# Kernel optimization log

Measured on AMD Instinct MI355X. Metric: run time of the kernel, lower is better.

The kernel has to match this reference:

```python
import jax, jax.numpy as jnp
import numpy as np

B, S, D = 24, 512, 512
H, HS, HSEL = 8, 1, 2
DK = D // H
DFF = 2048
NQ, NPID = 1000, 5000
NB = 2
NL = 3 * NB  # blocks_1 (NB) + blocks_2 (2*NB)
FC1, FC2 = 512, 256


def setup_inputs():
    key = jax.random.key(0)
    ks = jax.random.split(key, 32)
    def w(k, shape, scale=0.02):
        return jax.random.normal(k, shape, dtype=jnp.float32) * scale
    inp = {}
    inp['q_data'] = jax.random.randint(ks[0], (B, S), 0, NQ + 1)
    inp['target'] = jax.random.randint(ks[1], (B, S), 0, 2)
    inp['pid_data'] = jax.random.randint(ks[2], (B, S), 0, NPID + 1)
    # embedding tables (padding_idx=0 -> zero row)
    inp['q_embed_tab'] = w(ks[3], (NQ + 1, D)).at[0].set(0.0)
    inp['qa_embed_tab'] = w(ks[4], (3, D)).at[0].set(0.0)
    inp['q_diff_tab'] = w(ks[5], (NQ + 1, D)).at[0].set(0.0)
    inp['qa_diff_tab'] = w(ks[6], (2 * NQ + 1, D)).at[0].set(0.0)
    inp['pid_diff_tab'] = w(ks[7], (NPID + 1, 1)).at[0].set(0.0)
    # stacked per-layer transformer params, leading dim NL
    inp['Wq'] = w(ks[8], (NL, D, D)); inp['bq'] = jnp.zeros((NL, D), jnp.float32)
    inp['Wv'] = w(ks[9], (NL, D, D)); inp['bv'] = jnp.zeros((NL, D), jnp.float32)
    inp['Wg'] = w(ks[10], (NL, D, H - HS))  # router, no bias
    inp['Wo'] = w(ks[11], (NL, D, D)); inp['bo'] = jnp.zeros((NL, D), jnp.float32)
    inp['ln1_g'] = jnp.ones((NL, D), jnp.float32); inp['ln1_b'] = jnp.zeros((NL, D), jnp.float32)
    inp['W1'] = w(ks[12], (NL, D, DFF)); inp['b1'] = jnp.zeros((NL, DFF), jnp.float32)
    inp['W2'] = w(ks[13], (NL, DFF, D)); inp['b2'] = jnp.zeros((NL, D), jnp.float32)
    inp['ln2_g'] = jnp.ones((NL, D), jnp.float32); inp['ln2_b'] = jnp.zeros((NL, D), jnp.float32)
    # output MLP
    inp['ow1'] = w(ks[14], (2 * D, FC1)); inp['ob1'] = jnp.zeros((FC1,), jnp.float32)
    inp['ow2'] = w(ks[15], (FC1, FC2)); inp['ob2'] = jnp.zeros((FC2,), jnp.float32)
    inp['ow3'] = w(ks[16], (FC2, 1)); inp['ob3'] = jnp.zeros((1,), jnp.float32)
    return inp


def _ln(x, g, b, eps=1e-5):
    m = x.mean(-1, keepdims=True)
    v = ((x - m) ** 2).mean(-1, keepdims=True)
    return (x - m) * jax.lax.rsqrt(v + eps) * g + b


def _moh_attn(xq, xv, strict, Wq, bq, Wv, bv, Wg, Wo, bo):
    b, s, d = xq.shape
    ql = xq @ Wq + bq            # [b,s,D]; kq_same=True so k == q
    vl = xv @ Wv + bv
    q = ql.reshape(b, s, H, DK).transpose(0, 2, 1, 3)   # [b,H,s,dk]
    v = vl.reshape(b, s, H, DK).transpose(0, 2, 1, 3)
    scores = jnp.einsum('bhid,bhjd->bhij', q, q) / np.float32(np.sqrt(DK))
    i = jnp.arange(s)[:, None]
    j = jnp.arange(s)[None, :]
    allowed = (j < i) if strict else (j <= i)
    scores = jnp.where(allowed, scores, jnp.float32(-1e9))
    scores = scores.at[:, :, 0, :].set(0.0)  # pad_zero row -> uniform softmax
    # dynamic per-token head routing on the query projection
    gates = jax.nn.softmax(ql @ Wg, axis=-1)             # [b,s,H-HS]
    idx = jax.lax.top_k(gates, HSEL)[1]                  # [b,s,HSEL]
    dyn_mask = jax.nn.one_hot(idx, H - HS, dtype=gates.dtype).sum(-2)
    dyn_scores = gates * dyn_mask
    rmask = jnp.concatenate([jnp.ones((b, s, HS), gates.dtype), dyn_scores], -1).mean(1)  # [b,H]
    attn = jax.nn.softmax(scores, axis=-1)
    ctx = jnp.einsum('bhij,bhjd->bhid', attn, v) * rmask[:, :, None, None]
    ctx = ctx.transpose(0, 2, 1, 3).reshape(b, s, d)
    return ctx @ Wo + bo


def _block(xq, xv, strict, p):
    a = _moh_attn(xq, xv, strict, *p[:7])
    x = _ln(xq + a, p[7], p[8])
    f = jnp.maximum(x @ p[9] + p[10], 0.0) @ p[11] + p[12]
    return _ln(x + f, p[13], p[14])


def reference(q_data, target, pid_data, q_embed_tab, qa_embed_tab, q_diff_tab,
              qa_diff_tab, pid_diff_tab, Wq, bq, Wv, bv, Wg, Wo, bo,
              ln1_g, ln1_b, W1, b1, W2, b2, ln2_g, ln2_b,
              ow1, ob1, ow2, ob2, ow3, ob3):
    # Rasch-style embeddings (separate_qa=False, n_pid>0)
    q_emb = q_embed_tab[q_data]
    qa_emb = qa_embed_tab[target] + q_emb
    pid_emb = pid_diff_tab[pid_data]          # [B,S,1]
    qd = q_diff_tab[q_data]
    q_emb = q_emb + pid_emb * qd
    qa_emb = qa_emb + pid_emb * (qa_diff_tab[target] + qd)
    stacks = (Wq, bq, Wv, bv, Wg, Wo, bo, ln1_g, ln1_b, W1, b1, W2, b2, ln2_g, ln2_b)
    def P(i):
        return tuple(a[i] for a in stacks)
    y, x = qa_emb, q_emb
    for i in range(NB):                       # blocks_1: mask=1 (causal incl self)
        y = _block(y, y, False, P(i))
    flag = True
    for jj in range(2 * NB):                  # blocks_2: alternate self / cross-with-y
        i = NB + jj
        if flag:
            x = _block(x, x, False, P(i)); flag = False
        else:
            x = _block(x, y, True, P(i)); flag = True
    h = jnp.concatenate([x, q_emb], -1)       # [B,S,2D]
    h = jnp.maximum(h @ ow1 + ob1, 0.0)
    h = jnp.maximum(h @ ow2 + ob2, 0.0)
    return jax.nn.sigmoid((h @ ow3 + ob3)[..., 0])  # [B,S]
```

## Files before the change

### kernel.cpp

```cpp
#include <hip/hip_runtime.h>
#include <math.h>

typedef unsigned short u16;
typedef unsigned int   u32;
typedef __attribute__((ext_vector_type(8))) short short8;
typedef __attribute__((ext_vector_type(4))) float f32x4;
typedef __attribute__((ext_vector_type(16))) float f32x16;

#define Bb 24
#define Ss 512
#define Dd 512
#define DFFf 2048

__device__ __forceinline__ u16 f2b(float f) {
  u32 u = __float_as_uint(f);
  u32 r = (u + 0x7fffu + ((u >> 16) & 1u)) >> 16;
  return (u16)r;
}
__device__ __forceinline__ float b2f(u32 h) { return __uint_as_float(h << 16); }
__device__ __forceinline__ void cvt8(uint4 p, float* d) {
  d[0]=b2f(p.x&0xffffu); d[1]=b2f(p.x>>16);
  d[2]=b2f(p.y&0xffffu); d[3]=b2f(p.y>>16);
  d[4]=b2f(p.z&0xffffu); d[5]=b2f(p.z>>16);
  d[6]=b2f(p.w&0xffffu); d[7]=b2f(p.w>>16);
}

__global__ __launch_bounds__(256) void trans_kernel(
    const float* __restrict__ src, u16* __restrict__ dst, int K, int N,
    int dstLayer, int rowBase)
{
  __shared__ float t[32][33];
  int n0 = blockIdx.x*32, k0 = blockIdx.y*32;
  const float* s = src + (size_t)blockIdx.z*K*N;
  u16* d = dst + (size_t)blockIdx.z*dstLayer;
  int c = threadIdx.x & 31, r = threadIdx.x >> 5;
  #pragma unroll
  for (int rr=r; rr<32; rr+=8) t[rr][c] = s[(size_t)(k0+rr)*N + n0 + c];
  __syncthreads();
  #pragma unroll
  for (int rr=r; rr<32; rr+=8) d[(size_t)(rowBase + n0+rr)*K + k0 + c] = f2b(t[c][rr]);
}

__global__ __launch_bounds__(256) void embed_kernel(
    const int* __restrict__ q_data, const int* __restrict__ target, const int* __restrict__ pid_data,
    const float* __restrict__ q_tab, const float* __restrict__ qa_tab,
    const float* __restrict__ qd_tab, const float* __restrict__ qad_tab,
    const float* __restrict__ pid_tab,
    float* __restrict__ xb, float* __restrict__ yb,
    u16* __restrict__ qebf, u16* __restrict__ ybf)
{
  int t = blockIdx.x;
  int qi = q_data[t], tg = target[t], pi = pid_data[t];
  float pd = pid_tab[pi];
  const float* qe  = q_tab  + (size_t)qi*Dd;
  const float* qa  = qa_tab + (size_t)tg*Dd;
  const float* qd  = qd_tab + (size_t)qi*Dd;
  const float* qad = qad_tab+ (size_t)tg*Dd;
  size_t base = (size_t)t*Dd;
  for (int d = threadIdx.x; d < Dd; d += 256) {
    float e = qe[d], dv = qd[d];
    float qv  = e + pd*dv;
    float qav = qa[d] + e + pd*(qad[d] + dv);
    xb[base+d] = qv;  qebf[base+d] = f2b(qv);
    yb[base+d] = qav; ybf[base+d]  = f2b(qav);
  }
}

__global__ __launch_bounds__(256) void embed_x_kernel(
    const int* __restrict__ q_data, const int* __restrict__ pid_data,
    const float* __restrict__ q_tab, const float* __restrict__ qd_tab,
    const float* __restrict__ pid_tab, float* __restrict__ xb)
{
  int t = blockIdx.x;
  int qi = q_data[t], pi = pid_data[t];
  float pd = pid_tab[pi];
  const float* qe = q_tab + (size_t)qi*Dd;
  const float* qd = qd_tab + (size_t)qi*Dd;
  size_t base = (size_t)t*Dd;
  for (int d = threadIdx.x; d < Dd; d += 256)
    xb[base+d] = qe[d] + pd*qd[d];
}

__global__ __launch_bounds__(256) void gemm_bf16_kernel(
    const u16* __restrict__ A, const u16* __restrict__ A2,
    const u16* __restrict__ Wt,
    const float* __restrict__ bias, const float* __restrict__ bias2,
    float* __restrict__ Cf, u16* __restrict__ Cb, u16* __restrict__ Cb2,
    int M, int N, int K, int ldA, int ldw, int act, int nsplit, float* rinit)
{
  __shared__ u16 As[3][128*32];
  __shared__ u16 Bs[3][128*32];
  if (rinit && blockIdx.x==0 && blockIdx.y==0 && threadIdx.x < 192)
    rinit[threadIdx.x] = ((threadIdx.x & 7)==0) ? 1.f : 0.f;
  int bm = blockIdx.y*128, bn = blockIdx.x*128;
  int wv = threadIdx.x >> 6, lane = threadIdx.x & 63;
  int wm = (wv & 1)*64, wn = (wv >> 1)*64;

  const char* gAa[2]; const char* gAb[2]; const char* gB[2];
  u32 ldsOff[2];
  #pragma unroll
  for (int t=0; t<2; t++) {
    int flat = wv*128 + t*64 + lane;
    int row = flat >> 2, c = flat & 3;
    int sr = (row & 3) ^ ((row >> 2) & 3);
    int cb = ((c ^ sr) * 16);
    gAa[t] = (const char*)A + ((size_t)(bm+row)*ldA)*2 + cb;
    gAb[t] = A2 ? ((const char*)A2 + ((size_t)(bm+row)*ldA)*2 + cb) : gAa[t];
    gB[t]  = (const char*)Wt + ((size_t)(bn+row)*ldw)*2 + cb;
    ldsOff[t] = (u32)(wv*128 + t*64)*16;
  }
  int selLim = A2 ? 512 : 0x7fffffff;
  int kmask  = A2 ? 511 : 0x7fffffff;

  f32x16 acc[2][2];
  #pragma unroll
  for (int i=0;i<2;i++)
    #pragma unroll
    for (int j=0;j<2;j++)
      #pragma unroll
      for (int r=0;r<16;r++) acc[i][j][r] = 0.f;

  int m32 = lane & 31, hi = lane >> 5;
  int sL = (m32 & 3) ^ ((m32 >> 2) & 3);

  auto stage = [&](int kt, int buf) {
    int k0 = kt*32;
    size_t offA = (size_t)(k0 & kmask)*2;
    size_t offB = (size_t)k0*2;
    #pragma unroll
    for (int t=0; t<2; t++) {
      const char* sa = ((k0 < selLim) ? gAa[t] : gAb[t]) + offA;
      __builtin_amdgcn_global_load_lds(
          (const __attribute__((address_space(1))) void*)sa,
          (__attribute__((address_space(3))) void*)((char*)As[buf] + ldsOff[t]), 16, 0, 0);
      __builtin_amdgcn_global_load_lds(
          (const __attribute__((address_space(1))) void*)(gB[t] + offB),
          (__attribute__((address_space(3))) void*)((char*)Bs[buf] + ldsOff[t]), 16, 0, 0);
    }
  };

  int nk = K >> 5;
  stage(0, 0);
  stage(1, 1);
  for (int t=0; t<nk; t++) {
    if (t+1 < nk) {
      asm volatile("s_waitcnt vmcnt(4)\ns_barrier" ::: "memory");
    } else {
      asm volatile("s_waitcnt vmcnt(0)\ns_barrier" ::: "memory");
    }
    int buf = t % 3;
    const u16* Ab   = As[buf];
    const u16* Bbuf = Bs[buf];
    short8 af[2][2], bfr[2][2];
    #pragma unroll
    for (int i=0;i<2;i++)
      #pragma unroll
      for (int kk=0;kk<2;kk++) {
        af[i][kk]  = *(const short8*)(Ab   + (wm + i*32 + m32)*32 + (((kk*2+hi) ^ sL)*8));
        bfr[i][kk] = *(const short8*)(Bbuf + (wn + i*32 + m32)*32 + (((kk*2+hi) ^ sL)*8));
      }
    if (t+2 < nk) stage(t+2, (t+2) % 3);
    #pragma unroll
    for (int kk=0;kk<2;kk++)
      #pragma unroll
      for (int i=0;i<2;i++)
        #pragma unroll
        for (int j=0;j<2;j++)
          acc[i][j] = __builtin_amdgcn_mfma_f32_32x32x16_bf16(af[i][kk], bfr[j][kk], acc[i][j], 0, 0, 0);
  }

  int hisel = (bias2 != nullptr) && (bn >= nsplit);
  const float* bse = hisel ? bias2 : bias;
  u16* outb = hisel ? Cb2 : Cb;
  int cb0 = hisel ? nsplit : 0;
  int strideOut = bias2 ? nsplit : N;

  #pragma unroll
  for (int i=0;i<2;i++) {
    #pragma unroll
    for (int rg=0;rg<16;rg++) {
      int row = bm + wm + i*32 + (rg&3) + 8*(rg>>2) + 4*hi;
      #pragma unroll
      for (int j=0;j<2;j++) {
        int col = bn + wn + j*32 + m32;
        float v = acc[i][j][rg];
        if (bse) v += bse[col - cb0];
        if (act) v = fmaxf(v, 0.f);
        if (Cf)   Cf[(size_t)row*strideOut + col - cb0] = v;
        if (outb) outb[(size_t)row*strideOut + col - cb0] = f2b(v);
      }
    }
  }
}

__global__ __launch_bounds__(256) void add_ln_kernel(
    const float* __restrict__ xa, const u16* __restrict__ xbb,
    const float* __restrict__ g, const float* __restrict__ bta,
    float* __restrict__ outf, u16* __restrict__ outb)
{
  int row = blockIdx.x*4 + (threadIdx.x >> 6);
  int lane = threadIdx.x & 63;
  size_t base = (size_t)row*Dd + lane*8;
  float4 a0 = *(const float4*)(xa + base);
  float4 a1 = *(const float4*)(xa + base + 4);
  uint4  bb = *(const uint4*)(xbb + base);
  float v[8]; cvt8(bb, v);
  v[0]+=a0.x; v[1]+=a0.y; v[2]+=a0.z; v[3]+=a0.w;
  v[4]+=a1.x; v[5]+=a1.y; v[6]+=a1.z; v[7]+=a1.w;
  float s = ((v[0]+v[1])+(v[2]+v[3])) + ((v[4]+v[5])+(v[6]+v[7]));
  #pragma unroll
  for (int o=32;o;o>>=1) s += __shfl_xor(s, o);
  float mean = s * (1.f/512.f);
  float q = 0.f;
  #pragma unroll
  for (int k=0;k<8;k++) { float d = v[k]-mean; v[k]=d; q += d*d; }
  #pragma unroll
  for (int o=32;o;o>>=1) q += __shfl_xor(q, o);
  float inv = rsqrtf(q * (1.f/512.f) + 1e-5f);
  float4 g0 = *(const float4*)(g + lane*8);
  float4 g1 = *(const float4*)(g + lane*8 + 4);
  float4 b0 = *(const float4*)(bta + lane*8);
  float4 b1 = *(const float4*)(bta + lane*8 + 4);
  float r[8];
  r[0]=v[0]*inv*g0.x+b0.x; r[1]=v[1]*inv*g0.y+b0.y;
  r[2]=v[2]*inv*g0.z+b0.z; r[3]=v[3]*inv*g0.w+b0.w;
  r[4]=v[4]*inv*g1.x+b1.x; r[5]=v[5]*inv*g1.y+b1.y;
  r[6]=v[6]*inv*g1.z+b1.z; r[7]=v[7]*inv*g1.w+b1.w;
  float4 o0 = {r[0],r[1],r[2],r[3]};
  float4 o1 = {r[4],r[5],r[6],r[7]};
  *(float4*)(outf + base) = o0;
  *(float4*)(outf + base + 4) = o1;
  uint4 w;
  w.x = (u32)f2b(r[0]) | ((u32)f2b(r[1])<<16);
  w.y = (u32)f2b(r[2]) | ((u32)f2b(r[3])<<16);
  w.z = (u32)f2b(r[4]) | ((u32)f2b(r[5])<<16);
  w.w = (u32)f2b(r[6]) | ((u32)f2b(r[7])<<16);
  *(uint4*)(outb + base) = w;
}

__global__ __launch_bounds__(64) void router_kernel(
    const u16* __restrict__ ql, const float* __restrict__ Wg, float* __restrict__ rmask)
{
  int b = blockIdx.x >> 3, seg = blockIdx.x & 7;
  int lane = threadIdx.x;
  int s = seg*64 + lane;
  const u16* q = ql + ((size_t)b*Ss + s)*Dd;
  float lg[7];
  #pragma unroll
  for (int k=0;k<7;k++) lg[k]=0.f;
  for (int d0=0; d0<Dd; d0+=8) {
    uint4 p = *(const uint4*)(q+d0);
    float qa[8]; cvt8(p, qa);
    #pragma unroll
    for (int i=0;i<8;i++)
      #pragma unroll
      for (int k=0;k<7;k++) lg[k] += qa[i]*Wg[(d0+i)*7+k];
  }
  float mx = lg[0];
  #pragma unroll
  for (int k=1;k<7;k++) mx = fmaxf(mx, lg[k]);
  float sum = 0.f, gt[7];
  #pragma unroll
  for (int k=0;k<7;k++){ gt[k]=__expf(lg[k]-mx); sum+=gt[k]; }
  float invs = 1.f/sum;
  #pragma unroll
  for (int k=0;k<7;k++) gt[k]*=invs;
  int i1=0; float v1=gt[0];
  #pragma unroll
  for (int k=1;k<7;k++) if (gt[k]>v1){v1=gt[k]; i1=k;}
  int i2=-1; float v2=-1e30f;
  #pragma unroll
  for (int k=0;k<7;k++) if (k!=i1 && gt[k]>v2){v2=gt[k]; i2=k;}
  #pragma unroll
  for (int k=0;k<7;k++) {
    float d = (k==i1 || k==i2) ? gt[k] : 0.f;
    #pragma unroll
    for (int o=32;o;o>>=1) d += __shfl_down(d,o);
    if (lane==0) atomicAdd(&rmask[b*8 + 1 + k], d * (1.f/512.f));
  }
}

__global__ __launch_bounds__(256) void attn_mfma_kernel(
    const u16* __restrict__ ql, const u16* __restrict__ vl,
    const float* __restrict__ rmask, u16* __restrict__ ctx, int strict)
{
  __shared__ u16 Ks[64*64];
  __shared__ u16 Vts[64*64];
  __shared__ u16 Pw[4][32*72];
  int qt = blockIdx.x;
  int b = blockIdx.y >> 3, h = blockIdx.y & 7;
  int tid = threadIdx.x;

  if (qt == 4) {
    int d = tid & 63, seg = tid >> 6;
    const u16* vp = vl + (size_t)(b*Ss + seg*128)*Dd + h*64 + d;
    float s = 0.f;
    #pragma unroll 4
    for (int j=0; j<128; j++) s += b2f(vp[(size_t)j*Dd]);
    float* red = (float*)Ks;
    red[seg*64 + d] = s;
    __syncthreads();
    if (seg == 0) {
      float tot = red[d] + red[64+d] + red[128+d] + red[192+d];
      ctx[(size_t)b*Ss*Dd + h*64 + d] = f2b(tot * rmask[b*8+h] * (1.f/512.f));
    }
    return;
  }

  int wv = tid >> 6, lane = tid & 63;
  int mrow = lane & 15, quad = lane >> 4;

  int rowbase[2];
  rowbase[0] = qt*128 + wv*16;
  rowbase[1] = rowbase[0] + 64;

  short8 qf[2][2];
  #pragma unroll
  for (int i=0;i<2;i++)
    #pragma unroll
    for (int kf=0;kf<2;kf++)
      qf[i][kf] = *(const short8*)(ql + (size_t)(b*Ss + rowbase[i] + mrow)*Dd + h*64 + kf*32 + quad*8);

  f32x4 O[2][4];
  f32x4 L[2];
  #pragma unroll
  for (int i=0;i<2;i++) {
    L[i] = (f32x4){0.f,0.f,0.f,0.f};
    #pragma unroll
    for (int df=0;df<4;df++) O[i][df] = (f32x4){0.f,0.f,0.f,0.f};
  }
  short8 ones;
  #pragma unroll
  for (int z=0;z<8;z++) ones[z] = (short)0x3F80;

  int nt = 2*qt + 2;
  for (int t=0; t<nt; t++) {
    int j0 = t*64;
    __syncthreads();
    #pragma unroll
    for (int s2=0; s2<2; s2++) {
      int c = s2*256 + tid;
      int r = c >> 3, o = c & 7;
      uint4 kq = *(const uint4*)(ql + (size_t)(b*Ss + j0 + r)*Dd + h*64 + o*8);
      *(uint4*)(Ks + r*64 + ((o ^ (r&7))*8)) = kq;
    }
    {
      int j = tid & 63, d0 = (tid >> 6) * 16;
      const u16* vp = vl + (size_t)(b*Ss + j0 + j)*Dd + h*64 + d0;
      uint4 va = *(const uint4*)vp;
      uint4 vb = *(const uint4*)(vp + 8);
      u16 vals[16];
      vals[0]=(u16)va.x;  vals[1]=(u16)(va.x>>16);
      vals[2]=(u16)va.y;  vals[3]=(u16)(va.y>>16);
      vals[4]=(u16)va.z;  vals[5]=(u16)(va.z>>16);
      vals[6]=(u16)va.w;  vals[7]=(u16)(va.w>>16);
      vals[8]=(u16)vb.x;  vals[9]=(u16)(vb.x>>16);
      vals[10]=(u16)vb.y; vals[11]=(u16)(vb.y>>16);
      vals[12]=(u16)vb.z; vals[13]=(u16)(vb.z>>16);
      vals[14]=(u16)vb.w; vals[15]=(u16)(vb.w>>16);
      int jg = j >> 3, jo = j & 7;
      #pragma unroll
      for (int dd=0; dd<16; dd++) {
        int d = d0 + dd;
        Vts[d*64 + ((jg ^ (d&7))*8) + jo] = vals[dd];
      }
    }
    __syncthreads();

    f32x4 s[2][4];
    #pragma unroll
    for (int n=0;n<4;n++) {
      int r = n*16 + mrow, rs = r & 7;
      short8 kb0 = *(const short8*)(Ks + r*64 + ((quad  ^ rs))*8);
      short8 kb1 = *(const short8*)(Ks + r*64 + (((quad+4) ^ rs))*8);
      #pragma unroll
      for (int i=0;i<2;i++) {
        f32x4 a = (f32x4){0.f,0.f,0.f,0.f};
        a = __builtin_amdgcn_mfma_f32_16x16x32_bf16(qf[i][0], kb0, a, 0, 0, 0);
        a = __builtin_amdgcn_mfma_f32_16x16x32_bf16(qf[i][1], kb1, a, 0, 0, 0);
        s[i][n] = a;
      }
    }
    #pragma unroll
    for (int i=0;i<2;i++) {
      int rb = rowbase[i] + quad*4 - strict;
      #pragma unroll
      for (int n=0;n<4;n++) {
        int j = j0 + n*16 + mrow;
        #pragma unroll
        for (int r=0;r<4;r++) {
          float v = s[i][n][r]*0.125f;
          float p = (j <= rb + r) ? __expf(fminf(v, 60.f)) : 0.f;
          Pw[wv][(i*16 + quad*4 + r)*72 + n*16 + mrow] = f2b(p);
        }
      }
    }
    asm volatile("s_waitcnt lgkmcnt(0)" ::: "memory");
    short8 pf[2][2];
    #pragma unroll
    for (int pi=0; pi<2; pi++)
      #pragma unroll
      for (int kk=0; kk<2; kk++)
        pf[pi][kk] = *(const short8*)(&Pw[wv][(pi*16 + mrow)*72 + kk*32 + quad*8]);
    #pragma unroll
    for (int i=0;i<2;i++) {
      L[i] = __builtin_amdgcn_mfma_f32_16x16x32_bf16(pf[i][0], ones, L[i], 0, 0, 0);
      L[i] = __builtin_amdgcn_mfma_f32_16x16x32_bf16(pf[i][1], ones, L[i], 0, 0, 0);
    }
    #pragma unroll
    for (int df=0; df<4; df++) {
      int r = df*16 + mrow, rs = r & 7;
      short8 vb0 = *(const short8*)(Vts + r*64 + ((quad ^ rs))*8);
      short8 vb1 = *(const short8*)(Vts + r*64 + (((quad+4) ^ rs))*8);
      #pragma unroll
      for (int i=0;i<2;i++) {
        O[i][df] = __builtin_amdgcn_mfma_f32_16x16x32_bf16(pf[i][0], vb0, O[i][df], 0, 0, 0);
        O[i][df] = __builtin_amdgcn_mfma_f32_16x16x32_bf16(pf[i][1], vb1, O[i][df], 0, 0, 0);
      }
    }
  }

  float rm = rmask[b*8+h];
  #pragma unroll
  for (int i=0;i<2;i++) {
    #pragma unroll
    for (int r=0;r<4;r++) {
      int grow = rowbase[i] + quad*4 + r;
      if (grow != 0) {
        float sc = rm / L[i][r];
        u16* op = ctx + (size_t)(b*Ss + grow)*Dd + h*64 + mrow;
        #pragma unroll
        for (int df=0;df<4;df++)
          op[df*16] = f2b(O[i][df][r]*sc);
      }
    }
  }
}

__global__ __launch_bounds__(256) void head_kernel(
    const float* __restrict__ m2, const float* __restrict__ ow3, const float* __restrict__ ob3,
    float* __restrict__ out)
{
  int wave = threadIdx.x >> 6, lane = threadIdx.x & 63;
  int t = blockIdx.x*4 + wave;
  const float* r = m2 + (size_t)t*256;
  float s = 0.f;
  #pragma unroll
  for (int c=0;c<4;c++) s += r[lane + c*64] * ow3[lane + c*64];
  #pragma unroll
  for (int o=32;o;o>>=1) s += __shfl_down(s,o);
  if (lane==0) out[t] = 1.f/(1.f + __expf(-(s + ob3[0])));
}

static inline void gemmb(const u16* A, const u16* A2, const u16* Wt,
                         const float* b1_, const float* b2_,
                         float* Cf, u16* Cb, u16* Cb2,
                         int M, int N, int K, int ldA, int ldw, int act, int nsplit,
                         float* rinit, hipStream_t s) {
  gemm_bf16_kernel<<<dim3(N/128, M/128), 256, 0, s>>>(
      A, A2, Wt, b1_, b2_, Cf, Cb, Cb2, M, N, K, ldA, ldw, act, nsplit, rinit);
}

extern "C" void kernel_launch(void* const* d_in, const int* in_sizes, int n_in,
                              void* d_out, int out_size, void* d_ws, size_t ws_size,
                              hipStream_t stream) {
  const int*   q_data  = (const int*)d_in[0];
  const int*   target  = (const int*)d_in[1];
  const int*   pid_data= (const int*)d_in[2];
  const float* q_tab   = (const float*)d_in[3];
  const float* qa_tab  = (const float*)d_in[4];
  const float* qd_tab  = (const float*)d_in[5];
  const float* qad_tab = (const float*)d_in[6];
  const float* pid_tab = (const float*)d_in[7];
  const float* Wq = (const float*)d_in[8];
  const float* bq = (const float*)d_in[9];
  const float* Wv = (const float*)d_in[10];
  const float* bv = (const float*)d_in[11];
  const float* Wg = (const float*)d_in[12];
  const float* Wo = (const float*)d_in[13];
  const float* bo = (const float*)d_in[14];
  const float* ln1_g = (const float*)d_in[15];
  const float* ln1_b = (const float*)d_in[16];
  const float* W1 = (const float*)d_in[17];
  const float* b1 = (const float*)d_in[18];
  const float* W2 = (const float*)d_in[19];
  const float* b2 = (const float*)d_in[20];
  const float* ln2_g = (const float*)d_in[21];
  const float* ln2_b = (const float*)d_in[22];
  const float* ow1 = (const float*)d_in[23];
  const float* ob1 = (const float*)d_in[24];
  const float* ow2 = (const float*)d_in[25];
  const float* ob2 = (const float*)d_in[26];
  const float* ow3 = (const float*)d_in[27];
  const float* ob3 = (const float*)d_in[28];

  const size_t F = (size_t)Bb*Ss*Dd;
  float* ws = (float*)d_ws;
  float* Ax = ws;
  float* By = ws + F;
  float* Dt = ws + 2*F;
  u16* us = (u16*)(ws + 3*F);
  u16* Gy = us;
  u16* Hc = us + F;
  u16* Iq = us + 2*F;
  u16* Fx = us + 3*F;
  u16* Jq = us + 4*F;
  u16* Kv = us + 5*F;
  u16* Ma = us + 6*F;
  u16* wb = us + 7*F;
  u16* FFh = Fx;

  u16* WqvT = wb;
  u16* WoT  = WqvT + (size_t)6*1024*512;
  u16* W1T  = WoT  + (size_t)6*512*512;
  u16* W2T  = W1T  + (size_t)6*2048*512;
  u16* o1T  = W2T  + (size_t)6*512*2048;
  u16* o2T  = o1T  + (size_t)512*1024;
  float* rmaskb = (float*)(o2T + (size_t)256*512);

  const int M = Bb*Ss;

  trans_kernel<<<dim3(16,16,6), 256, 0, stream>>>(Wq, WqvT, 512, 512, 1024*512, 0);
  trans_kernel<<<dim3(16,16,6), 256, 0, stream>>>(Wv, WqvT, 512, 512, 1024*512, 512);
  trans_kernel<<<dim3(16,16,6), 256, 0, stream>>>(Wo, WoT, 512, 512, 512*512, 0);
  trans_kernel<<<dim3(64,16,6), 256, 0, stream>>>(W1, W1T, 512, 2048, 2048*512, 0);
  trans_kernel<<<dim3(16,64,6), 256, 0, stream>>>(W2, W2T, 2048, 512, 512*2048, 0);
  trans_kernel<<<dim3(16,32,1), 256, 0, stream>>>(ow1, o1T, 1024, 512, 0, 0);
  trans_kernel<<<dim3(8,16,1),  256, 0, stream>>>(ow2, o2T, 512, 256, 0, 0);

  embed_kernel<<<M, 256, 0, stream>>>(q_data, target, pid_data, q_tab, qa_tab,
                                      qd_tab, qad_tab, pid_tab, Ax, By, Iq, Gy);

  for (int l=0; l<6; l++) {
    int strict = (l==3||l==5) ? 1 : 0;
    const u16* Qbf  = (l<2) ? Gy : (l==2 ? Iq : Fx);
    const u16* Xvbf = (l<2) ? Gy : ((l==3||l==5) ? Gy : (l==4 ? Fx : Iq));
    float* Qf   = (l<2) ? By : Ax;
    float* x1f  = (l<2) ? Ax : By;
    u16*   Qout = (l<2) ? Gy : Fx;

    if (l==2)
      embed_x_kernel<<<M, 256, 0, stream>>>(q_data, pid_data, q_tab, qd_tab, pid_tab, Ax);

    const u16* WqvL = WqvT + (size_t)l*1024*512;
    if (!strict) {
      gemmb(Qbf, nullptr, WqvL, bq + l*512, bv + l*512, nullptr, Jq, Kv,
            M, 1024, 512, 512, 512, 0, 512, rmaskb, stream);
    } else {
      gemmb(Qbf,  nullptr, WqvL,                   bq + l*512, nullptr, nullptr, Jq, nullptr,
            M, 512, 512, 512, 512, 0, 512, rmaskb, stream);
      gemmb(Xvbf, nullptr, WqvL + (size_t)512*512, bv + l*512, nullptr, nullptr, Kv, nullptr,
            M, 512, 512, 512, 512, 0, 512, nullptr, stream);
    }
    router_kernel<<<Bb*8, 64, 0, stream>>>(Jq, Wg + (size_t)l*512*7, rmaskb);
    attn_mfma_kernel<<<dim3(5, Bb*8), 256, 0, stream>>>(Jq, Kv, rmaskb, Hc, strict);
    gemmb(Hc, nullptr, WoT + (size_t)l*512*512, bo + l*512, nullptr, nullptr, Ma, nullptr,
          M, 512, 512, 512, 512, 0, 512, nullptr, stream);
    add_ln_kernel<<<M/4, 256, 0, stream>>>(Qf, Ma, ln1_g + l*512, ln1_b + l*512, x1f, Hc);
    gemmb(Hc, nullptr, W1T + (size_t)l*2048*512, b1 + l*2048, nullptr,
          nullptr, FFh, nullptr, M, 2048, 512, 512, 512, 1, 2048, nullptr, stream);
    gemmb(FFh, nullptr, W2T + (size_t)l*512*2048, b2 + l*512, nullptr,
          nullptr, (u16*)Dt, nullptr, M, 512, 2048, 2048, 2048, 0, 512, nullptr, stream);
    add_ln_kernel<<<M/4, 256, 0, stream>>>(x1f, (u16*)Dt, ln2_g + l*512, ln2_b + l*512, Qf, Qout);
  }

  gemmb(Fx, Iq, o1T, ob1, nullptr, nullptr, Jq, nullptr,
        M, 512, 1024, 512, 1024, 1, 512, nullptr, stream);
  gemmb(Jq, nullptr, o2T, ob2, nullptr, (float*)Kv, nullptr, nullptr,
        M, 256, 512, 512, 512, 1, 256, nullptr, stream);
  head_kernel<<<M/4, 256, 0, stream>>>((float*)Kv, ow3, ob3, (float*)d_out);
}
```

Before: 1.954 ms.

## Template GEMM on M-tile size, use 256-row tiles and fuse strict Q/V projections

Templates the bf16 GEMM on the M tile (128 or 256 rows). The 256-row variant gives each wave a 64x128 output slab so every B fragment is reused across more rows. A new amode selects a per-N-half A source, so the strict layers' separate Q and V projections become one launch. The attention kernel's probability conversion to bf16 now truncates instead of rounding to nearest even. Larger tiles raise register and LDS use and cut the number of workgroups, which may lower occupancy and leave some CUs idle.

Measured after the change: 2.552 ms. 1.31x slower.

```diff
diff --git a/kernel.cpp b/kernel.cpp
--- a/kernel.cpp
+++ b/kernel.cpp
@@ -81,42 +81,57 @@
     xb[base+d] = qe[d] + pd*qd[d];
 }
 
+template<int MR>
 __global__ __launch_bounds__(256) void gemm_bf16_kernel(
     const u16* __restrict__ A, const u16* __restrict__ A2,
     const u16* __restrict__ Wt,
     const float* __restrict__ bias, const float* __restrict__ bias2,
     float* __restrict__ Cf, u16* __restrict__ Cb, u16* __restrict__ Cb2,
-    int M, int N, int K, int ldA, int ldw, int act, int nsplit, float* rinit)
-{
-  __shared__ u16 As[3][128*32];
+    int M, int N, int K, int ldA, int ldw, int act, int nsplit, int amode,
+    float* rinit)
+{
+  constexpr int TA = MR/64;
+  constexpr int BJ = MR/64;
+  __shared__ u16 As[3][MR*32];
   __shared__ u16 Bs[3][128*32];
   if (rinit && blockIdx.x==0 && blockIdx.y==0 && threadIdx.x < 192)
     rinit[threadIdx.x] = ((threadIdx.x & 7)==0) ? 1.f : 0.f;
-  int bm = blockIdx.y*128, bn = blockIdx.x*128;
+  int bm = blockIdx.y*MR, bn = blockIdx.x*128;
   int wv = threadIdx.x >> 6, lane = threadIdx.x & 63;
-  int wm = (wv & 1)*64, wn = (wv >> 1)*64;
-
-  const char* gAa[2]; const char* gAb[2]; const char* gB[2];
-  u32 ldsOff[2];
-  #pragma unroll
-  for (int t=0; t<2; t++) {
-    int flat = wv*128 + t*64 + lane;
+  int wm, wn;
+  if (MR == 256) { wm = wv*64; wn = 0; }
+  else           { wm = (wv & 1)*64; wn = (wv >> 1)*64; }
+
+  const u16* Abase = (amode==2 && bn >= nsplit) ? A2 : A;
+
+  const char* gAa[TA]; const char* gAb[TA]; const char* gB[2];
+  u32 ldsOffA[TA]; u32 ldsOffB[2];
+  #pragma unroll
+  for (int t=0; t<TA; t++) {
+    int flat = t*256 + wv*64 + lane;
     int row = flat >> 2, c = flat & 3;
     int sr = (row & 3) ^ ((row >> 2) & 3);
     int cb = ((c ^ sr) * 16);
-    gAa[t] = (const char*)A + ((size_t)(bm+row)*ldA)*2 + cb;
-    gAb[t] = A2 ? ((const char*)A2 + ((size_t)(bm+row)*ldA)*2 + cb) : gAa[t];
-    gB[t]  = (const char*)Wt + ((size_t)(bn+row)*ldw)*2 + cb;
-    ldsOff[t] = (u32)(wv*128 + t*64)*16;
-  }
-  int selLim = A2 ? 512 : 0x7fffffff;
-  int kmask  = A2 ? 511 : 0x7fffffff;
-
-  f32x16 acc[2][2];
+    gAa[t] = (const char*)Abase + ((size_t)(bm+row)*ldA)*2 + cb;
+    gAb[t] = (amode==1) ? ((const char*)A2 + ((size_t)(bm+row)*ldA)*2 + cb) : gAa[t];
+    ldsOffA[t] = (u32)(t*256 + wv*64)*16;
+  }
+  #pragma unroll
+  for (int t=0; t<2; t++) {
+    int flat = t*256 + wv*64 + lane;
+    int row = flat >> 2, c = flat & 3;
+    int sr = (row & 3) ^ ((row >> 2) & 3);
+    int cb = ((c ^ sr) * 16);
+    gB[t] = (const char*)Wt + ((size_t)(bn+row)*ldw)*2 + cb;
+    ldsOffB[t] = (u32)(t*256 + wv*64)*16;
+  }
+  int kmask = (amode==1) ? 511 : 0x7fffffff;
+
+  f32x16 acc[2][BJ];
   #pragma unroll
   for (int i=0;i<2;i++)
     #pragma unroll
-    for (int j=0;j<2;j++)
+    for (int j=0;j<BJ;j++)
       #pragma unroll
       for (int r=0;r<16;r++) acc[i][j][r] = 0.f;
 
@@ -128,15 +143,17 @@
     size_t offA = (size_t)(k0 & kmask)*2;
     size_t offB = (size_t)k0*2;
     #pragma unroll
-    for (int t=0; t<2; t++) {
-      const char* sa = ((k0 < selLim) ? gAa[t] : gAb[t]) + offA;
+    for (int t=0; t<TA; t++) {
+      const char* sa = ((amode==1 && k0 >= 512) ? gAb[t] : gAa[t]) + offA;
       __builtin_amdgcn_global_load_lds(
           (const __attribute__((address_space(1))) void*)sa,
-          (__attribute__((address_space(3))) void*)((char*)As[buf] + ldsOff[t]), 16, 0, 0);
+          (__attribute__((address_space(3))) void*)((char*)As[buf] + ldsOffA[t]), 16, 0, 0);
+    }
+    #pragma unroll
+    for (int t=0; t<2; t++)
       __builtin_amdgcn_global_load_lds(
           (const __attribute__((address_space(1))) void*)(gB[t] + offB),
-          (__attribute__((address_space(3))) void*)((char*)Bs[buf] + ldsOff[t]), 16, 0, 0);
-    }
+          (__attribute__((address_space(3))) void*)((char*)Bs[buf] + ldsOffB[t]), 16, 0, 0);
   };
 
   int nk = K >> 5;
@@ -144,28 +161,32 @@
   stage(1, 1);
   for (int t=0; t<nk; t++) {
     if (t+1 < nk) {
-      asm volatile("s_waitcnt vmcnt(4)\ns_barrier" ::: "memory");
+      if (MR == 256) asm volatile("s_waitcnt vmcnt(6)\ns_barrier" ::: "memory");
+      else           asm volatile("s_waitcnt vmcnt(4)\ns_barrier" ::: "memory");
     } else {
       asm volatile("s_waitcnt vmcnt(0)\ns_barrier" ::: "memory");
     }
     int buf = t % 3;
     const u16* Ab   = As[buf];
     const u16* Bbuf = Bs[buf];
-    short8 af[2][2], bfr[2][2];
+    short8 af[2][2], bfr[BJ][2];
     #pragma unroll
     for (int i=0;i<2;i++)
       #pragma unroll
-      for (int kk=0;kk<2;kk++) {
-        af[i][kk]  = *(const short8*)(Ab   + (wm + i*32 + m32)*32 + (((kk*2+hi) ^ sL)*8));
-        bfr[i][kk] = *(const short8*)(Bbuf + (wn + i*32 + m32)*32 + (((kk*2+hi) ^ sL)*8));
-      }
+      for (int kk=0;kk<2;kk++)
+        af[i][kk]  = *(const short8*)(Ab + (wm + i*32 + m32)*32 + (((kk*2+hi) ^ sL)*8));
+    #pragma unroll
+    for (int j=0;j<BJ;j++)
+      #pragma unroll
+      for (int kk=0;kk<2;kk++)
+        bfr[j][kk] = *(const short8*)(Bbuf + (wn + j*32 + m32)*32 + (((kk*2+hi) ^ sL)*8));
     if (t+2 < nk) stage(t+2, (t+2) % 3);
     #pragma unroll
     for (int kk=0;kk<2;kk++)
       #pragma unroll
       for (int i=0;i<2;i++)
         #pragma unroll
-        for (int j=0;j<2;j++)
+        for (int j=0;j<BJ;j++)
           acc[i][j] = __builtin_amdgcn_mfma_f32_32x32x16_bf16(af[i][kk], bfr[j][kk], acc[i][j], 0, 0, 0);
   }
 
@@ -181,7 +202,7 @@
     for (int rg=0;rg<16;rg++) {
       int row = bm + wm + i*32 + (rg&3) + 8*(rg>>2) + 4*hi;
       #pragma unroll
-      for (int j=0;j<2;j++) {
+      for (int j=0;j<BJ;j++) {
         int col = bn + wn + j*32 + m32;
         float v = acc[i][j][rg];
         if (bse) v += bse[col - cb0];
@@ -391,7 +412,7 @@
         for (int r=0;r<4;r++) {
           float v = s[i][n][r]*0.125f;
           float p = (j <= rb + r) ? __expf(fminf(v, 60.f)) : 0.f;
-          Pw[wv][(i*16 + quad*4 + r)*72 + n*16 + mrow] = f2b(p);
+          Pw[wv][(i*16 + quad*4 + r)*72 + n*16 + mrow] = (u16)(__float_as_uint(p) >> 16);
         }
       }
     }
@@ -452,13 +473,21 @@
   if (lane==0) out[t] = 1.f/(1.f + __expf(-(s + ob3[0])));
 }
 
-static inline void gemmb(const u16* A, const u16* A2, const u16* Wt,
-                         const float* b1_, const float* b2_,
-                         float* Cf, u16* Cb, u16* Cb2,
-                         int M, int N, int K, int ldA, int ldw, int act, int nsplit,
-                         float* rinit, hipStream_t s) {
-  gemm_bf16_kernel<<<dim3(N/128, M/128), 256, 0, s>>>(
-      A, A2, Wt, b1_, b2_, Cf, Cb, Cb2, M, N, K, ldA, ldw, act, nsplit, rinit);
+static inline void gemm128(const u16* A, const u16* A2, const u16* Wt,
+                           const float* b1_, const float* b2_,
+                           float* Cf, u16* Cb, u16* Cb2,
+                           int M, int N, int K, int ldA, int ldw, int act,
+                           int nsplit, int amode, float* rinit, hipStream_t s) {
+  gemm_bf16_kernel<128><<<dim3(N/128, M/128), 256, 0, s>>>(
+      A, A2, Wt, b1_, b2_, Cf, Cb, Cb2, M, N, K, ldA, ldw, act, nsplit, amode, rinit);
+}
+static inline void gemm256(const u16* A, const u16* A2, const u16* Wt,
+                           const float* b1_, const float* b2_,
+                           float* Cf, u16* Cb, u16* Cb2,
+                           int M, int N, int K, int ldA, int ldw, int act,
+                           int nsplit, int amode, float* rinit, hipStream_t s) {
+  gemm_bf16_kernel<256><<<dim3(N/128, M/256), 256, 0, s>>>(
+      A, A2, Wt, b1_, b2_, Cf, Cb, Cb2, M, N, K, ldA, ldw, act, nsplit, amode, rinit);
 }
 
 extern "C" void kernel_launch(void* const* d_in, const int* in_sizes, int n_in,
@@ -543,30 +572,24 @@
       embed_x_kernel<<<M, 256, 0, stream>>>(q_data, pid_data, q_tab, qd_tab, pid_tab, Ax);
 
     const u16* WqvL = WqvT + (size_t)l*1024*512;
-    if (!strict) {
-      gemmb(Qbf, nullptr, WqvL, bq + l*512, bv + l*512, nullptr, Jq, Kv,
-            M, 1024, 512, 512, 512, 0, 512, rmaskb, stream);
-    } else {
-      gemmb(Qbf,  nullptr, WqvL,                   bq + l*512, nullptr, nullptr, Jq, nullptr,
-            M, 512, 512, 512, 512, 0, 512, rmaskb, stream);
-      gemmb(Xvbf, nullptr, WqvL + (size_t)512*512, bv + l*512, nullptr, nullptr, Kv, nullptr,
-            M, 512, 512, 512, 512, 0, 512, nullptr, stream);
-    }
+    gemm256(Qbf, strict ? Xvbf : nullptr, WqvL, bq + l*512, bv + l*512,
+            nullptr, Jq, Kv, M, 1024, 512, 512, 512, 0, 512,
+            strict ? 2 : 0, rmaskb, stream);
     router_kernel<<<Bb*8, 64, 0, stream>>>(Jq, Wg + (size_t)l*512*7, rmaskb);
     attn_mfma_kernel<<<dim3(5, Bb*8), 256, 0, stream>>>(Jq, Kv, rmaskb, Hc, strict);
-    gemmb(Hc, nullptr, WoT + (size_t)l*512*512, bo + l*512, nullptr, nullptr, Ma, nullptr,
-          M, 512, 512, 512, 512, 0, 512, nullptr, stream);
+    gemm128(Hc, nullptr, WoT + (size_t)l*512*512, bo + l*512, nullptr,
+            nullptr, Ma, nullptr, M, 512, 512, 512, 512, 0, 512, 0, nullptr, stream);
     add_ln_kernel<<<M/4, 256, 0, stream>>>(Qf, Ma, ln1_g + l*512, ln1_b + l*512, x1f, Hc);
-    gemmb(Hc, nullptr, W1T + (size_t)l*2048*512, b1 + l*2048, nullptr,
-          nullptr, FFh, nullptr, M, 2048, 512, 512, 512, 1, 2048, nullptr, stream);
-    gemmb(FFh, nullptr, W2T + (size_t)l*512*2048, b2 + l*512, nullptr,
-          nullptr, (u16*)Dt, nullptr, M, 512, 2048, 2048, 2048, 0, 512, nullptr, stream);
+    gemm256(Hc, nullptr, W1T + (size_t)l*2048*512, b1 + l*2048, nullptr,
+            nullptr, FFh, nullptr, M, 2048, 512, 512, 512, 1, 2048, 0, nullptr, stream);
+    gemm256(FFh, nullptr, W2T + (size_t)l*512*2048, b2 + l*512, nullptr,
+            nullptr, (u16*)Dt, nullptr, M, 512, 2048, 2048, 2048, 0, 512, 0, nullptr, stream);
     add_ln_kernel<<<M/4, 256, 0, stream>>>(x1f, (u16*)Dt, ln2_g + l*512, ln2_b + l*512, Qf, Qout);
   }
 
-  gemmb(Fx, Iq, o1T, ob1, nullptr, nullptr, Jq, nullptr,
-        M, 512, 1024, 512, 1024, 1, 512, nullptr, stream);
-  gemmb(Jq, nullptr, o2T, ob2, nullptr, (float*)Kv, nullptr, nullptr,
-        M, 256, 512, 512, 512, 1, 256, nullptr, stream);
+  gemm256(Fx, Iq, o1T, ob1, nullptr, nullptr, Jq, nullptr,
+          M, 512, 1024, 512, 1024, 1, 512, 1, nullptr, stream);
+  gemm128(Jq, nullptr, o2T, ob2, nullptr, (float*)Kv, nullptr, nullptr,
+          M, 256, 512, 512, 512, 1, 256, 0, nullptr, stream);
   head_kernel<<<M/4, 256, 0, stream>>>((float*)Kv, ow3, ob3, (float*)d_out);
 }
```
